# Performance work log

Measured on AMD Instinct MI355X. Metric: run time of the kernel, lower is better.

## Reference

```python
import jax, jax.numpy as jnp
import numpy as np

WH, WW = 7, 7
N = WH * WW
DIM = 384
HEADS = 12
NW = 64          # windows per image
B_ = 2048        # batch * NW


def _relative_position_index():
    ch, cw = np.meshgrid(np.arange(WH), np.arange(WW), indexing='ij')
    coords = np.stack([ch, cw]).reshape(2, -1)                      # [2, N]
    rel = coords[:, :, None] - coords[:, None, :]                   # [2, N, N]
    rel = rel.transpose(1, 2, 0)
    rel[:, :, 0] += WH - 1
    rel[:, :, 1] += WW - 1
    rel[:, :, 0] *= 2 * WW - 1
    return jnp.asarray(rel.sum(-1), dtype=jnp.int32)                # [N, N]


def setup_inputs() -> dict:
    key = jax.random.key(0)
    ks = jax.random.split(key, 7)
    return {
        'x': jax.random.normal(ks[0], (B_, N, DIM), dtype=jnp.float32),
        'qkv_w': jax.random.normal(ks[1], (3 * DIM, DIM), dtype=jnp.float32) * 0.02,
        'qkv_b': jax.random.normal(ks[2], (3 * DIM,), dtype=jnp.float32) * 0.02,
        'proj_w': jax.random.normal(ks[3], (DIM, DIM), dtype=jnp.float32) * 0.02,
        'proj_b': jax.random.normal(ks[4], (DIM,), dtype=jnp.float32) * 0.02,
        'bias_table': jax.random.normal(ks[5], ((2 * WH - 1) * (2 * WW - 1), HEADS), dtype=jnp.float32) * 0.02,
        'mask': jax.random.normal(ks[6], (NW, N, N), dtype=jnp.float32),
        'rel_idx': _relative_position_index(),
    }


def reference(x, qkv_w, qkv_b, proj_w, proj_b, bias_table, mask, rel_idx):
    B_, n, C = x.shape
    H = HEADS
    hd = C // H
    scale = hd ** (-0.5)

    qkv = x @ qkv_w.T + qkv_b                                        # [B_, N, 3C]
    qkv = qkv.reshape(B_, n, 3, H, hd).transpose(2, 0, 3, 1, 4)      # [3, B_, H, N, hd]
    q, k, v = qkv[0], qkv[1], qkv[2]

    attn = jnp.einsum('bhqd,bhkd->bhqk', q * scale, k)               # [B_, H, N, N]

    rpb = bias_table[rel_idx.reshape(-1)].reshape(n, n, H)           # gather [N, N, H]
    attn = attn + rpb.transpose(2, 0, 1)[None]                       # [B_, H, N, N]

    nW = mask.shape[0]
    attn = attn.reshape(B_ // nW, nW, H, n, n) + mask[None, :, None]
    attn = attn.reshape(B_, H, n, n)
    attn = jax.nn.softmax(attn, axis=-1)

    out = jnp.einsum('bhqk,bhkd->bhqd', attn, v)                     # [B_, H, N, hd]
    out = out.transpose(0, 2, 1, 3).reshape(B_, n, C)
    return out @ proj_w.T + proj_b
```

## Files before the change

### kernel.cpp

```cpp
#include <hip/hip_runtime.h>
#include <hip/hip_bf16.h>
#include <cstdint>
#include <cstddef>

#define NTOK 49
#define DIM 384
#define KDIM 384
#define HEADS 12
#define HD 32
#define BATCH 2048
#define MROWS (BATCH * NTOK)

typedef unsigned short u16;
typedef __bf16 bf16x8 __attribute__((ext_vector_type(8)));
typedef unsigned short u16x8 __attribute__((ext_vector_type(8)));
typedef float f32x4 __attribute__((ext_vector_type(4)));
typedef float f32x16 __attribute__((ext_vector_type(16)));

__device__ __forceinline__ u16 f2b(float f) {
  union { float f; unsigned u; } v; v.f = f;
  unsigned r = v.u + 0x7fffu + ((v.u >> 16) & 1u);
  return (u16)(r >> 16);
}

__device__ __forceinline__ bf16x8 ld_bf8(const u16* p) {
  u16x8 u = *(const u16x8*)p;
  return __builtin_bit_cast(bf16x8, u);
}

__device__ __forceinline__ void gload_lds16(const void* g, void* l) {
  __builtin_amdgcn_global_load_lds(
      (const __attribute__((address_space(1))) unsigned*)g,
      (__attribute__((address_space(3))) unsigned*)l, 16, 0, 0);
}

__global__ __launch_bounds__(256) void k_prep(const float* __restrict__ x,
                                              u16* __restrict__ xb,
                                              const float* __restrict__ qkv_w,
                                              u16* __restrict__ wqkvb,
                                              const float* __restrict__ proj_w,
                                              u16* __restrict__ wprojb,
                                              const float* __restrict__ bias_table,
                                              const float* __restrict__ mask,
                                              const int* __restrict__ rel_idx,
                                              float* __restrict__ rpbm) {
  int blk = blockIdx.x;
  if (blk < 38208) {
    const float* in;
    u16* out;
    int i;
    if (blk < 37632) {
      in = x; out = xb; i = blk * 256 + threadIdx.x;
    } else if (blk < 38064) {
      in = qkv_w; out = wqkvb; i = (blk - 37632) * 256 + threadIdx.x;
    } else {
      in = proj_w; out = wprojb; i = (blk - 38064) * 256 + threadIdx.x;
    }
    float4 v = ((const float4*)in)[i];
    ushort4 o;
    o.x = f2b(v.x); o.y = f2b(v.y); o.z = f2b(v.z); o.w = f2b(v.w);
    ((ushort4*)out)[i] = o;
  } else {
    int gidx = (blk - 38208) * 256 + threadIdx.x;
    int l    = gidx & 63;
    int rq   = (gidx >> 6) & 3;
    int tile = (gidx >> 8) & 3;
    int w    = (gidx >> 10) & 63;
    int h    = gidx >> 16;
    int mi = tile >> 1, nj = tile & 1;
    int kk0 = mi * 32 + 8 * rq + 4 * (l >> 5);
    int qq  = nj * 32 + (l & 31);
    float4 out;
    float* op = (float*)&out;
#pragma unroll
    for (int rl = 0; rl < 4; ++rl) {
      int kk = kk0 + rl;
      float v = -1e30f;
      if (kk < NTOK && qq < NTOK)
        v = bias_table[rel_idx[qq * NTOK + kk] * HEADS + h] +
            mask[(w * NTOK + qq) * NTOK + kk];
      op[rl] = v;
    }
    ((float4*)rpbm)[gidx] = out;
  }
}

template <int OUT_BF16, int NCOLS, int NTN, int GD8>
__global__ __launch_bounds__(512, 4) void k_gemm256(const u16* __restrict__ A,
                                                    const u16* __restrict__ B,
                                                    const float* __restrict__ bias,
                                                    void* __restrict__ Cv) {
  __shared__ u16 sh[36864];
  int bid = blockIdx.x;
  int tile = (bid & 7) * GD8 + (bid >> 3);
  int mt = tile / NTN, nt = tile - mt * NTN;
  long m0 = (long)mt * 256;
  int n0 = nt * 128;
  int tid = threadIdx.x;
  int lane = tid & 63, wid = tid >> 6;
  int wr = (wid >> 1) * 64, wc = (wid & 1) * 64;
  int c = lane & 15, g = lane >> 4;
  int gsw = (g ^ ((c >> 1) & 3)) * 8;

  int srow = wid * 16 + (lane >> 2);
  int scol = ((lane & 3) ^ ((lane >> 3) & 3)) * 8;
  const u16* gA = A + (m0 + srow) * (long)KDIM + scol;
  const u16* gB = B + (long)(n0 + srow) * KDIM + scol;
  int lrow = srow, lseg = (lane & 3) * 8;

  f32x4 acc[4][4] = {};
  bf16x8 af[4], bfr[4];

#define STAGE256(BUF, KT)                                                      \
  {                                                                            \
    u16* As_ = sh + (BUF) * 12288;                                             \
    u16* Bs_ = As_ + 8192;                                                     \
    gload_lds16(gA + (KT), &As_[lrow * 32 + lseg]);                            \
    gload_lds16(gA + (KT) + 128L * KDIM, &As_[(lrow + 128) * 32 + lseg]);      \
    gload_lds16(gB + (KT), &Bs_[lrow * 32 + lseg]);                            \
  }

#define FRAGREAD(BUF)                                                          \
  {                                                                            \
    const u16* As = sh + (BUF) * 12288;                                        \
    const u16* Bs = As + 8192;                                                 \
    _Pragma("unroll") for (int i = 0; i < 4; ++i) {                            \
      af[i]  = ld_bf8(&As[(wr + i * 16 + c) * 32 + gsw]);                      \
      bfr[i] = ld_bf8(&Bs[(wc + i * 16 + c) * 32 + gsw]);                      \
    }                                                                          \
  }

#define MFMA_CL                                                                \
  __builtin_amdgcn_s_setprio(1);                                               \
  _Pragma("unroll") for (int mi = 0; mi < 4; ++mi)                             \
  _Pragma("unroll") for (int ni = 0; ni < 4; ++ni)                             \
      acc[mi][ni] = __builtin_amdgcn_mfma_f32_16x16x32_bf16(                   \
          af[mi], bfr[ni], acc[mi][ni], 0, 0, 0);                              \
  __builtin_amdgcn_s_setprio(0);

#define GITER(T, NV)                                                           \
  {                                                                            \
    MFMA_CL;                                                                   \
    asm volatile("s_waitcnt vmcnt(" #NV ")" ::: "memory");                     \
    __builtin_amdgcn_s_barrier();                                              \
    __builtin_amdgcn_sched_barrier(0);                                         \
    if ((T) + 3 < 12) STAGE256((T) % 3, ((T) + 3) * 32);                       \
    FRAGREAD(((T) + 1) % 3);                                                   \
  }

  STAGE256(0, 0);
  STAGE256(1, 32);
  STAGE256(2, 64);
  asm volatile("s_waitcnt vmcnt(6)" ::: "memory");
  __builtin_amdgcn_s_barrier();
  __builtin_amdgcn_sched_barrier(0);
  FRAGREAD(0);

  GITER(0, 3)  GITER(1, 3)  GITER(2, 3)  GITER(3, 3)
  GITER(4, 3)  GITER(5, 3)  GITER(6, 3)  GITER(7, 3)
  GITER(8, 3)  GITER(9, 3)  GITER(10, 0)
  { MFMA_CL; }
  __builtin_amdgcn_s_barrier();
#undef GITER
#undef MFMA_CL
#undef FRAGREAD
#undef STAGE256

  if (OUT_BF16) {
    u16* C = (u16*)Cv;
#pragma unroll
    for (int mi = 0; mi < 4; ++mi)
#pragma unroll
      for (int ni = 0; ni < 4; ++ni) {
        int col = wc + ni * 16 + c;
        float bv = bias[n0 + col];
#pragma unroll
        for (int r = 0; r < 4; ++r) {
          int row = wr + mi * 16 + g * 4 + r;
          sh[row * 128 + col] = f2b(acc[mi][ni][r] + bv);
        }
      }
    __syncthreads();
#pragma unroll
    for (int rep = 0; rep < 8; ++rep) {
      int idx = rep * 4096 + tid * 8;
      int row = idx >> 7, col = idx & 127;
      int grow = (int)m0 + row;
      int b = grow / 49, tok = grow - b * 49;
      int gcol = n0 + col;
      int t = gcol / 384;
      int hc = gcol - t * 384;
      int h = hc >> 5, d0 = hc & 31;
      size_t off = (((size_t)(t * 12 + h) * BATCH + b) * 49 + tok) * 32 + d0;
      *(u16x8*)(C + off) = *(const u16x8*)&sh[idx];
    }
  } else {
    float* C = (float*)Cv;
    float* shf = (float*)sh;
#pragma unroll
    for (int chunk = 0; chunk < 2; ++chunk) {
      __syncthreads();
      if ((wid >> 2) == chunk) {
#pragma unroll
        for (int mi = 0; mi < 4; ++mi)
#pragma unroll
          for (int ni = 0; ni < 4; ++ni) {
            int col = wc + ni * 16 + c;
            float bv = bias[n0 + col];
#pragma unroll
            for (int r = 0; r < 4; ++r) {
              int lr = ((wid >> 1) & 1) * 64 + mi * 16 + g * 4 + r;
              shf[lr * 128 + col] = acc[mi][ni][r] + bv;
            }
          }
      }
      __syncthreads();
#pragma unroll
      for (int rep = 0; rep < 8; ++rep) {
        int idx = rep * 2048 + tid * 4;
        int row = idx >> 7, col = idx & 127;
        *(float4*)(C + (m0 + chunk * 128 + row) * NCOLS + n0 + col) =
            *(const float4*)&shf[idx];
      }
    }
  }
}

__global__ __launch_bounds__(256, 4) void k_attn(const u16* __restrict__ qkv,
                                                 const float* __restrict__ rpbmT,
                                                 u16* __restrict__ attnout) {
  int lane = threadIdx.x & 63, wid = threadIdx.x >> 6;
  int blk0 = blockIdx.x;
  int blk = (blk0 & 7) * 768 + (blk0 >> 3);
  int w = blk / 96;
  int rr = blk - w * 96;
  int j = rr / 3;
  int hb = rr - j * 3;
  int b = j * 64 + w;
  int h = hb * 4 + wid;
  int l31 = lane & 31, hi = lane >> 5;

  const u16* qh = qkv + ((size_t)(h)*BATCH + b) * (49 * 32);
  const u16* kh = qkv + ((size_t)(12 + h) * BATCH + b) * (49 * 32);
  const u16* vh = qkv + ((size_t)(24 + h) * BATCH + b) * (49 * 32);

  bf16x8 kf[2][2], qf[2][2];
#pragma unroll
  for (int mi = 0; mi < 2; ++mi) {
    int row = mi * 32 + l31; if (row > NTOK - 1) row = NTOK - 1;
#pragma unroll
    for (int k2 = 0; k2 < 2; ++k2)
      kf[mi][k2] = ld_bf8(kh + row * 32 + k2 * 16 + hi * 8);
  }
#pragma unroll
  for (int nj = 0; nj < 2; ++nj) {
    int row = nj * 32 + l31; if (row > NTOK - 1) row = NTOK - 1;
#pragma unroll
    for (int k2 = 0; k2 < 2; ++k2)
      qf[nj][k2] = ld_bf8(qh + row * 32 + k2 * 16 + hi * 8);
  }

  f32x16 s[2][2];
  f32x16 z16 = {};
#pragma unroll
  for (int mi = 0; mi < 2; ++mi)
#pragma unroll
    for (int nj = 0; nj < 2; ++nj) {
      s[mi][nj] = __builtin_amdgcn_mfma_f32_32x32x16_bf16(kf[mi][0], qf[nj][0],
                                                          z16, 0, 0, 0);
      s[mi][nj] = __builtin_amdgcn_mfma_f32_32x32x16_bf16(kf[mi][1], qf[nj][1],
                                                          s[mi][nj], 0, 0, 0);
    }

  const float scale = 0.17677669529663687f;
  const f32x4* rp = (const f32x4*)(rpbmT + ((size_t)(h * 64 + w)) * 4096);
#pragma unroll
  for (int mi = 0; mi < 2; ++mi)
#pragma unroll
    for (int nj = 0; nj < 2; ++nj)
#pragma unroll
      for (int rq = 0; rq < 4; ++rq) {
        f32x4 rv = rp[(mi * 2 + nj) * 256 + rq * 64 + lane];
#pragma unroll
        for (int rl = 0; rl < 4; ++rl)
          s[mi][nj][rq * 4 + rl] = s[mi][nj][rq * 4 + rl] * scale + rv[rl];
      }

#pragma unroll
  for (int nj = 0; nj < 2; ++nj) {
    float mx = s[0][nj][0];
#pragma unroll
    for (int mi = 0; mi < 2; ++mi)
#pragma unroll
      for (int r = 0; r < 16; ++r)
        mx = fmaxf(mx, s[mi][nj][r]);
    mx = fmaxf(mx, __shfl_xor(mx, 32));
    float sum = 0.f;
#pragma unroll
    for (int mi = 0; mi < 2; ++mi)
#pragma unroll
      for (int r = 0; r < 16; ++r) {
        float p = __expf(s[mi][nj][r] - mx);
        s[mi][nj][r] = p;
        sum += p;
      }
    sum += __shfl_xor(sum, 32);
    float inv = __builtin_amdgcn_rcpf(sum);
#pragma unroll
    for (int mi = 0; mi < 2; ++mi)
#pragma unroll
      for (int r = 0; r < 16; ++r)
        s[mi][nj][r] *= inv;
  }

  f32x16 o[2] = {};
#pragma unroll
  for (int kk = 0; kk < 4; ++kk) {
    u16x8 tmp;
#pragma unroll
    for (int e = 0; e < 8; ++e)
      tmp[e] = vh[(kk * 16 + hi * 8 + e) * 32 + l31];
    bf16x8 vbk = __builtin_bit_cast(bf16x8, tmp);
#pragma unroll
    for (int nj = 0; nj < 2; ++nj) {
      const int mi = kk >> 1, br = (kk & 1) * 8;
      unsigned t0, t1, t2, t3;
      asm("v_cvt_pk_bf16_f32 %0, %1, %2"
          : "=v"(t0) : "v"(s[mi][nj][br + 0]), "v"(s[mi][nj][br + 1]));
      asm("v_cvt_pk_bf16_f32 %0, %1, %2"
          : "=v"(t1) : "v"(s[mi][nj][br + 2]), "v"(s[mi][nj][br + 3]));
      asm("v_cvt_pk_bf16_f32 %0, %1, %2"
          : "=v"(t2) : "v"(s[mi][nj][br + 4]), "v"(s[mi][nj][br + 5]));
      asm("v_cvt_pk_bf16_f32 %0, %1, %2"
          : "=v"(t3) : "v"(s[mi][nj][br + 6]), "v"(s[mi][nj][br + 7]));
      asm("v_permlane32_swap_b32 %0, %1" : "+v"(t0), "+v"(t2));
      asm("v_permlane32_swap_b32 %0, %1" : "+v"(t1), "+v"(t3));
      uint4 uu; uu.x = t0; uu.y = t1; uu.z = t2; uu.w = t3;
      bf16x8 pa = __builtin_bit_cast(bf16x8, uu);
      o[nj] = __builtin_amdgcn_mfma_f32_32x32x16_bf16(pa, vbk, o[nj], 0, 0, 0);
    }
  }

  u16* obase = attnout + (size_t)b * (NTOK * DIM) + h * HD;
#pragma unroll
  for (int nj = 0; nj < 2; ++nj)
#pragma unroll
    for (int r = 0; r < 16; ++r) {
      int q = nj * 32 + (r & 3) + 8 * (r >> 2) + 4 * hi;
      if (q < NTOK)
        obase[(size_t)q * DIM + l31] = f2b(o[nj][r]);
    }
}

extern "C" void kernel_launch(void* const* d_in, const int* in_sizes, int n_in,
                              void* d_out, int out_size, void* d_ws, size_t ws_size,
                              hipStream_t stream) {
  const float* x       = (const float*)d_in[0];
  const float* qkv_w   = (const float*)d_in[1];
  const float* qkv_b   = (const float*)d_in[2];
  const float* proj_w  = (const float*)d_in[3];
  const float* proj_b  = (const float*)d_in[4];
  const float* bias_tb = (const float*)d_in[5];
  const float* mask    = (const float*)d_in[6];
  const int*   rel_idx = (const int*)d_in[7];
  float* out = (float*)d_out;

  char* ws = (char*)d_ws;
  u16*   xb      = (u16*)(ws + 0);
  u16*   wqkvb   = (u16*)(ws + 77070336);
  u16*   wprojb  = (u16*)(ws + 77955072);
  float* rpbm    = (float*)(ws + 78249984);
  u16*   qkv     = (u16*)(ws + 90832896);
  u16*   attnout = (u16*)(ws + 322043904);

  k_prep<<<41280, 256, 0, stream>>>(x, xb, qkv_w, wqkvb, proj_w, wprojb,
                                    bias_tb, mask, rel_idx, rpbm);

  k_gemm256<1, 1152, 9, 441><<<3528, 512, 0, stream>>>(xb, wqkvb, qkv_b,
                                                       (void*)qkv);

  k_attn<<<6144, 256, 0, stream>>>(qkv, rpbm, attnout);

  k_gemm256<0, 384, 3, 147><<<1176, 512, 0, stream>>>(attnout, wprojb, proj_b,
                                                      (void*)out);

  (void)in_sizes; (void)n_in; (void)out_size; (void)ws_size;
}
```

Before: 340.7 us.

## Fuse fp32-to-bf16 conversion of x into QKV GEMM A-tile loading

Measured after the change: 488.3 us. 1.43x slower.

```diff
diff --git a/kernel.cpp b/kernel.cpp
--- a/kernel.cpp
+++ b/kernel.cpp
@@ -34,9 +34,13 @@
       (__attribute__((address_space(3))) unsigned*)l, 16, 0, 0);
 }
 
-__global__ __launch_bounds__(256) void k_prep(const float* __restrict__ x,
-                                              u16* __restrict__ xb,
-                                              const float* __restrict__ qkv_w,
+__device__ __forceinline__ unsigned pkbf(float lo, float hi) {
+  unsigned r;
+  asm("v_cvt_pk_bf16_f32 %0, %1, %2" : "=v"(r) : "v"(lo), "v"(hi));
+  return r;
+}
+
+__global__ __launch_bounds__(256) void k_prep(const float* __restrict__ qkv_w,
                                               u16* __restrict__ wqkvb,
                                               const float* __restrict__ proj_w,
                                               u16* __restrict__ wprojb,
@@ -45,23 +49,18 @@
                                               const int* __restrict__ rel_idx,
                                               float* __restrict__ rpbm) {
   int blk = blockIdx.x;
-  if (blk < 38208) {
+  if (blk < 576) {
     const float* in;
     u16* out;
     int i;
-    if (blk < 37632) {
-      in = x; out = xb; i = blk * 256 + threadIdx.x;
-    } else if (blk < 38064) {
-      in = qkv_w; out = wqkvb; i = (blk - 37632) * 256 + threadIdx.x;
-    } else {
-      in = proj_w; out = wprojb; i = (blk - 38064) * 256 + threadIdx.x;
-    }
+    if (blk < 432) { in = qkv_w; out = wqkvb; i = blk * 256 + threadIdx.x; }
+    else           { in = proj_w; out = wprojb; i = (blk - 432) * 256 + threadIdx.x; }
     float4 v = ((const float4*)in)[i];
     ushort4 o;
     o.x = f2b(v.x); o.y = f2b(v.y); o.z = f2b(v.z); o.w = f2b(v.w);
     ((ushort4*)out)[i] = o;
   } else {
-    int gidx = (blk - 38208) * 256 + threadIdx.x;
+    int gidx = (blk - 576) * 256 + threadIdx.x;
     int l    = gidx & 63;
     int rq   = (gidx >> 6) & 3;
     int tile = (gidx >> 8) & 3;
@@ -85,11 +84,147 @@
   }
 }
 
-template <int OUT_BF16, int NCOLS, int NTN, int GD8>
+__global__ __launch_bounds__(512, 4) void k_gemmqkv(const float* __restrict__ Xf,
+                                                    const u16* __restrict__ B,
+                                                    const float* __restrict__ bias,
+                                                    u16* __restrict__ C) {
+  __shared__ u16 sh[36864];
+  int bid = blockIdx.x;
+  int tile = (bid & 7) * 441 + (bid >> 3);
+  int mt = tile / 9, nt = tile - mt * 9;
+  long m0 = (long)mt * 256;
+  int n0 = nt * 128;
+  int tid = threadIdx.x;
+  int lane = tid & 63, wid = tid >> 6;
+  int wr = (wid >> 1) * 64, wc = (wid & 1) * 64;
+  int c = lane & 15, g = lane >> 4;
+  int gsw = (g ^ ((c >> 1) & 3)) * 8;
+
+  int srow = wid * 16 + (lane >> 2);
+  int scol = ((lane & 3) ^ ((lane >> 3) & 3)) * 8;
+  const u16* gB = B + (long)(n0 + srow) * KDIM + scol;
+  int lrow = srow, lseg = (lane & 3) * 8;
+
+  int ar = tid >> 1;
+  int ahf = tid & 1;
+  const float* gAf = Xf + (m0 + ar) * 384 + ahf * 16;
+  int aX = (ar >> 1) & 3;
+  int ap0 = (2 * ahf) ^ aX;
+  int ap1 = (2 * ahf + 1) ^ aX;
+  int abase = ar * 64;
+
+  f32x4 acc[4][4] = {};
+  bf16x8 af[4], bfr[4];
+  float4 a0, a1, a2, a3;
+
+#define ALOAD(KT)                                                              \
+  {                                                                            \
+    a0 = *(const float4*)(gAf + (KT));                                         \
+    a1 = *(const float4*)(gAf + (KT) + 4);                                     \
+    a2 = *(const float4*)(gAf + (KT) + 8);                                     \
+    a3 = *(const float4*)(gAf + (KT) + 12);                                    \
+  }
+
+#define AWRITE(BUF)                                                            \
+  {                                                                            \
+    char* Ab = (char*)sh + (BUF) * 24576;                                      \
+    uint4 w0, w1;                                                              \
+    w0.x = pkbf(a0.x, a0.y); w0.y = pkbf(a0.z, a0.w);                          \
+    w0.z = pkbf(a1.x, a1.y); w0.w = pkbf(a1.z, a1.w);                          \
+    w1.x = pkbf(a2.x, a2.y); w1.y = pkbf(a2.z, a2.w);                          \
+    w1.z = pkbf(a3.x, a3.y); w1.w = pkbf(a3.z, a3.w);                          \
+    *(uint4*)(Ab + abase + ap0 * 16) = w0;                                     \
+    *(uint4*)(Ab + abase + ap1 * 16) = w1;                                     \
+  }
+
+#define BSTAGE(BUF, KT)                                                        \
+  gload_lds16(gB + (KT), &sh[(BUF) * 12288 + 8192 + lrow * 32 + lseg]);
+
+#define FRAGREAD(BUF)                                                          \
+  {                                                                            \
+    const u16* As = sh + (BUF) * 12288;                                        \
+    const u16* Bs = As + 8192;                                                 \
+    _Pragma("unroll") for (int i = 0; i < 4; ++i) {                            \
+      af[i]  = ld_bf8(&As[(wr + i * 16 + c) * 32 + gsw]);                      \
+      bfr[i] = ld_bf8(&Bs[(wc + i * 16 + c) * 32 + gsw]);                      \
+    }                                                                          \
+  }
+
+#define MFMA_CL                                                                \
+  __builtin_amdgcn_s_setprio(1);                                               \
+  _Pragma("unroll") for (int mi = 0; mi < 4; ++mi)                             \
+  _Pragma("unroll") for (int ni = 0; ni < 4; ++ni)                             \
+      acc[mi][ni] = __builtin_amdgcn_mfma_f32_16x16x32_bf16(                   \
+          af[mi], bfr[ni], acc[mi][ni], 0, 0, 0);                              \
+  __builtin_amdgcn_s_setprio(0);
+
+#define GITERQ(T, NV)                                                          \
+  {                                                                            \
+    MFMA_CL;                                                                   \
+    asm volatile("s_waitcnt vmcnt(" #NV ") lgkmcnt(0)" ::: "memory");          \
+    __builtin_amdgcn_s_barrier();                                              \
+    __builtin_amdgcn_sched_barrier(0);                                         \
+    if ((T) + 2 < 12) AWRITE(((T) + 2) % 3);           \
+    if ((T) + 3 < 12) { ALOAD(((T) + 3) * 32); BSTAGE((T) % 3, ((T) + 3) * 32); } \
+    FRAGREAD(((T) + 1) % 3);                                                   \
+  }
+
+  ALOAD(0);  AWRITE(0);
+  ALOAD(32); AWRITE(1);
+  BSTAGE(0, 0);
+  BSTAGE(1, 32);
+  BSTAGE(2, 64);
+  ALOAD(64);
+  asm volatile("s_waitcnt vmcnt(6) lgkmcnt(0)" ::: "memory");
+  __builtin_amdgcn_s_barrier();
+  __builtin_amdgcn_sched_barrier(0);
+  FRAGREAD(0);
+
+  GITERQ(0, 5)  GITERQ(1, 5)  GITERQ(2, 5)  GITERQ(3, 5)
+  GITERQ(4, 5)  GITERQ(5, 5)  GITERQ(6, 5)  GITERQ(7, 5)
+  GITERQ(8, 5)  GITERQ(9, 5)  GITERQ(10, 0)
+  { MFMA_CL; }
+  __builtin_amdgcn_s_barrier();
+#undef GITERQ
+#undef MFMA_CL
+#undef FRAGREAD
+#undef BSTAGE
+#undef AWRITE
+#undef ALOAD
+
+#pragma unroll
+  for (int mi = 0; mi < 4; ++mi)
+#pragma unroll
+    for (int ni = 0; ni < 4; ++ni) {
+      int col = wc + ni * 16 + c;
+      float bv = bias[n0 + col];
+#pragma unroll
+      for (int r = 0; r < 4; ++r) {
+        int row = wr + mi * 16 + g * 4 + r;
+        sh[row * 128 + col] = f2b(acc[mi][ni][r] + bv);
+      }
+    }
+  __syncthreads();
+#pragma unroll
+  for (int rep = 0; rep < 8; ++rep) {
+    int idx = rep * 4096 + tid * 8;
+    int row = idx >> 7, col = idx & 127;
+    int grow = (int)m0 + row;
+    int b = grow / 49, tok = grow - b * 49;
+    int gcol = n0 + col;
+    int t = gcol / 384;
+    int hc = gcol - t * 384;
+    int h = hc >> 5, d0 = hc & 31;
+    size_t off = (((size_t)(t * 12 + h) * BATCH + b) * 49 + tok) * 32 + d0;
+    *(u16x8*)(C + off) = *(const u16x8*)&sh[idx];
+  }
+}
+
+template <int NTN, int GD8>
 __global__ __launch_bounds__(512, 4) void k_gemm256(const u16* __restrict__ A,
                                                     const u16* __restrict__ B,
                                                     const float* __restrict__ bias,
-                                                    void* __restrict__ Cv) {
+                                                    float* __restrict__ C) {
   __shared__ u16 sh[36864];
   int bid = blockIdx.x;
   int tile = (bid & 7) * GD8 + (bid >> 3);
@@ -166,62 +301,31 @@
 #undef FRAGREAD
 #undef STAGE256
 
-  if (OUT_BF16) {
-    u16* C = (u16*)Cv;
-#pragma unroll
-    for (int mi = 0; mi < 4; ++mi)
-#pragma unroll
-      for (int ni = 0; ni < 4; ++ni) {
-        int col = wc + ni * 16 + c;
-        float bv = bias[n0 + col];
-#pragma unroll
-        for (int r = 0; r < 4; ++r) {
-          int row = wr + mi * 16 + g * 4 + r;
-          sh[row * 128 + col] = f2b(acc[mi][ni][r] + bv);
+  float* shf = (float*)sh;
+#pragma unroll
+  for (int chunk = 0; chunk < 2; ++chunk) {
+    __syncthreads();
+    if ((wid >> 2) == chunk) {
+#pragma unroll
+      for (int mi = 0; mi < 4; ++mi)
+#pragma unroll
+        for (int ni = 0; ni < 4; ++ni) {
+          int col = wc + ni * 16 + c;
+          float bv = bias[n0 + col];
+#pragma unroll
+          for (int r = 0; r < 4; ++r) {
+            int lr = ((wid >> 1) & 1) * 64 + mi * 16 + g * 4 + r;
+            shf[lr * 128 + col] = acc[mi][ni][r] + bv;
+          }
         }
-      }
+    }
     __syncthreads();
 #pragma unroll
     for (int rep = 0; rep < 8; ++rep) {
-      int idx = rep * 4096 + tid * 8;
+      int idx = rep * 2048 + tid * 4;
       int row = idx >> 7, col = idx & 127;
-      int grow = (int)m0 + row;
-      int b = grow / 49, tok = grow - b * 49;
-      int gcol = n0 + col;
-      int t = gcol / 384;
-      int hc = gcol - t * 384;
-      int h = hc >> 5, d0 = hc & 31;
-      size_t off = (((size_t)(t * 12 + h) * BATCH + b) * 49 + tok) * 32 + d0;
-      *(u16x8*)(C + off) = *(const u16x8*)&sh[idx];
-    }
-  } else {
-    float* C = (float*)Cv;
-    float* shf = (float*)sh;
-#pragma unroll
-    for (int chunk = 0; chunk < 2; ++chunk) {
-      __syncthreads();
-      if ((wid >> 2) == chunk) {
-#pragma unroll
-        for (int mi = 0; mi < 4; ++mi)
-#pragma unroll
-          for (int ni = 0; ni < 4; ++ni) {
-            int col = wc + ni * 16 + c;
-            float bv = bias[n0 + col];
-#pragma unroll
-            for (int r = 0; r < 4; ++r) {
-              int lr = ((wid >> 1) & 1) * 64 + mi * 16 + g * 4 + r;
-              shf[lr * 128 + col] = acc[mi][ni][r] + bv;
-            }
-          }
-      }
-      __syncthreads();
-#pragma unroll
-      for (int rep = 0; rep < 8; ++rep) {
-        int idx = rep * 2048 + tid * 4;
-        int row = idx >> 7, col = idx & 127;
-        *(float4*)(C + (m0 + chunk * 128 + row) * NCOLS + n0 + col) =
-            *(const float4*)&shf[idx];
-      }
+      *(float4*)(C + (m0 + chunk * 128 + row) * 384 + n0 + col) =
+          *(const float4*)&shf[idx];
     }
   }
 }
@@ -324,15 +428,10 @@
 #pragma unroll
     for (int nj = 0; nj < 2; ++nj) {
       const int mi = kk >> 1, br = (kk & 1) * 8;
-      unsigned t0, t1, t2, t3;
-      asm("v_cvt_pk_bf16_f32 %0, %1, %2"
-          : "=v"(t0) : "v"(s[mi][nj][br + 0]), "v"(s[mi][nj][br + 1]));
-      asm("v_cvt_pk_bf16_f32 %0, %1, %2"
-          : "=v"(t1) : "v"(s[mi][nj][br + 2]), "v"(s[mi][nj][br + 3]));
-      asm("v_cvt_pk_bf16_f32 %0, %1, %2"
-          : "=v"(t2) : "v"(s[mi][nj][br + 4]), "v"(s[mi][nj][br + 5]));
-      asm("v_cvt_pk_bf16_f32 %0, %1, %2"
-          : "=v"(t3) : "v"(s[mi][nj][br + 6]), "v"(s[mi][nj][br + 7]));
+      unsigned t0 = pkbf(s[mi][nj][br + 0], s[mi][nj][br + 1]);
+      unsigned t1 = pkbf(s[mi][nj][br + 2], s[mi][nj][br + 3]);
+      unsigned t2 = pkbf(s[mi][nj][br + 4], s[mi][nj][br + 5]);
+      unsigned t3 = pkbf(s[mi][nj][br + 6], s[mi][nj][br + 7]);
       asm("v_permlane32_swap_b32 %0, %1" : "+v"(t0), "+v"(t2));
       asm("v_permlane32_swap_b32 %0, %1" : "+v"(t1), "+v"(t3));
       uint4 uu; uu.x = t0; uu.y = t1; uu.z = t2; uu.w = t3;
@@ -366,23 +465,20 @@
   float* out = (float*)d_out;
 
   char* ws = (char*)d_ws;
-  u16*   xb      = (u16*)(ws + 0);
+  u16*   attnout = (u16*)(ws + 0);
   u16*   wqkvb   = (u16*)(ws + 77070336);
   u16*   wprojb  = (u16*)(ws + 77955072);
   float* rpbm    = (float*)(ws + 78249984);
   u16*   qkv     = (u16*)(ws + 90832896);
-  u16*   attnout = (u16*)(ws + 322043904);
-
-  k_prep<<<41280, 256, 0, stream>>>(x, xb, qkv_w, wqkvb, proj_w, wprojb,
-                                    bias_tb, mask, rel_idx, rpbm);
-
-  k_gemm256<1, 1152, 9, 441><<<3528, 512, 0, stream>>>(xb, wqkvb, qkv_b,
-                                                       (void*)qkv);
+
+  k_prep<<<3648, 256, 0, stream>>>(qkv_w, wqkvb, proj_w, wprojb,
+                                   bias_tb, mask, rel_idx, rpbm);
+
+  k_gemmqkv<<<3528, 512, 0, stream>>>(x, wqkvb, qkv_b, qkv);
 
   k_attn<<<6144, 256, 0, stream>>>(qkv, rpbm, attnout);
 
-  k_gemm256<0, 384, 3, 147><<<1176, 512, 0, stream>>>(attnout, wprojb, proj_b,
-                                                      (void*)out);
+  k_gemm256<3, 147><<<1176, 512, 0, stream>>>(attnout, wprojb, proj_b, out);
 
   (void)in_sizes; (void)n_in; (void)out_size; (void)ws_size;
 }
```
